# Performance work log

Measured on AMD Instinct MI355X. Metric: run time of the kernel, lower is better.

Reference implementation:

```python
import jax, jax.numpy as jnp
import numpy as np

S, B, C, H = 1024, 4, 1024, 16
CC = C // H


def setup_inputs() -> dict:
    key = jax.random.key(0)
    ks = jax.random.split(key, 10)
    scale = 1.0 / np.sqrt(C)
    return {
        "x": jax.random.normal(ks[0], (S, B, C), dtype=jnp.float32),
        "r": jax.random.normal(ks[1], (S, B, C), dtype=jnp.float32),
        "Wq": jax.random.normal(ks[2], (C, C), dtype=jnp.float32) * scale,
        "bq": jnp.zeros((C,), dtype=jnp.float32),
        "Wke": jax.random.normal(ks[3], (C, C), dtype=jnp.float32) * scale,
        "bke": jnp.zeros((C,), dtype=jnp.float32),
        "Wkr": jax.random.normal(ks[4], (C, C), dtype=jnp.float32) * scale,
        "bkr": jnp.zeros((C,), dtype=jnp.float32),
        "u": jax.random.normal(ks[5], (C,), dtype=jnp.float32) * 0.02,
        "v": jax.random.normal(ks[6], (C,), dtype=jnp.float32) * 0.02,
    }


def reference(x, r, Wq, bq, Wke, bke, Wkr, bkr, u, v):
    s, b, c = x.shape
    h, cc = H, CC
    # projections (torch Linear: y = x @ W^T + b)
    ewq = (x @ Wq.T + bq).reshape(s, b, h, cc)
    ewke_full = x @ Wke.T + bke                 # [s,b,c]
    ewke = ewke_full.reshape(s, b, h, cc)
    rwkr_full = r @ Wkr.T + bkr                 # [s,b,c]
    rwkr = rwkr_full.reshape(s, b, h, cc)
    # content-content and content-position terms
    term_a = jnp.einsum('sbnc,tbnc->stbn', ewq, ewke)
    term_b = jnp.einsum('sbnc,tbnc->stbn', ewq, rwkr)
    # global bias terms: uwke/vwke are constant over (s,b), so the stb einsum
    # reduces to a tb contraction broadcast over s (same math, no s*b copies)
    uwke = Wke @ u + bke                        # [c]
    vwke = Wkr @ v + bkr                        # [c]
    term_c = jnp.einsum('c,tbc->tb', uwke, ewke_full)   # [t,b]
    term_d = jnp.einsum('c,tbc->tb', vwke, rwkr_full)   # [t,b]
    bias = (term_c + term_d)[None, :, :, None]          # [1,t,b,1]
    return term_a + term_b + bias               # [s,t,b,h]
```

## Files before the change

### kernel.cpp

```cpp
#include <hip/hip_runtime.h>
#include <hip/hip_bf16.h>
#include <stdint.h>

#define Ssz 1024
#define Bsz 4
#define Csz 1024
#define Hsz 16
#define Msz 4096

typedef unsigned short u16;
typedef __attribute__((ext_vector_type(8))) short bf16x8;
typedef __attribute__((ext_vector_type(8))) unsigned short u16x8;
typedef __attribute__((ext_vector_type(4))) float f32x4;
typedef __attribute__((ext_vector_type(4))) unsigned short u16x4;

__device__ __forceinline__ u16 f2bf(float f) {
  union { float f; unsigned u; } x; x.f = f;
  unsigned r = x.u + 0x7fffu + ((x.u >> 16) & 1u);
  return (u16)(r >> 16);
}

__device__ __forceinline__ void glds16(const void* g, void* l) {
  __builtin_amdgcn_global_load_lds(
      (__attribute__((address_space(1))) void*)g,
      (__attribute__((address_space(3))) void*)l, 16, 0, 0);
}

__device__ __forceinline__ int swzb(int x) { return x ^ (((x >> 8) & 7) << 4); }

__global__ __launch_bounds__(256) void k_convert_w(
    const float* __restrict__ Wq, const float* __restrict__ Wke, const float* __restrict__ Wkr,
    const float* __restrict__ bke, const float* __restrict__ bkr,
    const float* __restrict__ uu, const float* __restrict__ vv,
    u16* __restrict__ Bq, u16* __restrict__ B2, float* __restrict__ biasK,
    float* __restrict__ uwke, float* __restrict__ vwke) {
  int c = blockIdx.x;
  int tid = threadIdx.x;
  int c4 = tid * 4;
  float4 q = *(const float4*)(Wq + (size_t)c * Csz + c4);
  float4 e = *(const float4*)(Wke + (size_t)c * Csz + c4);
  float4 k = *(const float4*)(Wkr + (size_t)c * Csz + c4);
  u16x4 qo = { f2bf(q.x), f2bf(q.y), f2bf(q.z), f2bf(q.w) };
  u16x4 eo = { f2bf(e.x), f2bf(e.y), f2bf(e.z), f2bf(e.w) };
  u16x4 ko = { f2bf(k.x), f2bf(k.y), f2bf(k.z), f2bf(k.w) };
  *(u16x4*)(Bq + (size_t)c * 1024 + c4) = qo;
  *(u16x4*)(B2 + (size_t)c * 2048 + c4) = eo;
  *(u16x4*)(B2 + (size_t)c * 2048 + 1024 + c4) = ko;
  float4 u4 = *(const float4*)(uu + c4);
  float4 v4 = *(const float4*)(vv + c4);
  float se = e.x * u4.x + e.y * u4.y + e.z * u4.z + e.w * u4.w;
  float sk = k.x * v4.x + k.y * v4.y + k.z * v4.z + k.w * v4.w;
  for (int m = 32; m; m >>= 1) { se += __shfl_xor(se, m); sk += __shfl_xor(sk, m); }
  __shared__ float red[2][4];
  if ((tid & 63) == 0) { red[0][tid >> 6] = se; red[1][tid >> 6] = sk; }
  __syncthreads();
  if (tid == 0) {
    uwke[c] = red[0][0] + red[0][1] + red[0][2] + red[0][3] + bke[c];
    vwke[c] = red[1][0] + red[1][1] + red[1][2] + red[1][3] + bkr[c];
    biasK[c] = bke[c] + bkr[c];
  }
}

__global__ __launch_bounds__(256) void k_prep2(
    const float* __restrict__ Wke, const float* __restrict__ Wkr,
    const float* __restrict__ uwke, const float* __restrict__ vwke,
    const float* __restrict__ bke, const float* __restrict__ bkr,
    float* __restrict__ wu, float* __restrict__ wv, float* __restrict__ cst) {
  int bid = blockIdx.x;
  int tid = threadIdx.x;
  if (bid < 64) {
    const float* W = (bid < 32) ? Wke : Wkr;
    const float* sv = (bid < 32) ? uwke : vwke;
    float* o = (bid < 32) ? wu : wv;
    int d = (bid & 31) * 32 + (tid & 31);
    int cpar = tid >> 5;
    float acc = 0.f;
    #pragma unroll 8
    for (int c = cpar; c < Csz; c += 8) acc += sv[c] * W[(size_t)c * Csz + d];
    __shared__ float red[8][32];
    red[cpar][tid & 31] = acc;
    __syncthreads();
    if (cpar == 0) {
      float s = 0.f;
      #pragma unroll
      for (int i = 0; i < 8; i++) s += red[i][tid & 31];
      o[d] = s;
    }
  } else {
    float s = 0.f;
    for (int i = tid; i < Csz; i += 256) s += uwke[i] * bke[i] + vwke[i] * bkr[i];
    for (int m = 32; m; m >>= 1) s += __shfl_xor(s, m);
    __shared__ float red1[4];
    if ((tid & 63) == 0) red1[tid >> 6] = s;
    __syncthreads();
    if (tid == 0) cst[0] = red1[0] + red1[1] + red1[2] + red1[3];
  }
}

__global__ __launch_bounds__(256) void k_convert_xr_bias(
    const float* __restrict__ x, const float* __restrict__ r,
    const float* __restrict__ wu, const float* __restrict__ wv,
    const float* __restrict__ cst, u16* __restrict__ A2, float* __restrict__ biasTB) {
  int m = blockIdx.x;
  int tid = threadIdx.x;
  int c4 = tid * 4;
  float4 xv = *(const float4*)(x + (size_t)m * Csz + c4);
  float4 rv = *(const float4*)(r + (size_t)m * Csz + c4);
  u16x4 xo = { f2bf(xv.x), f2bf(xv.y), f2bf(xv.z), f2bf(xv.w) };
  u16x4 ro = { f2bf(rv.x), f2bf(rv.y), f2bf(rv.z), f2bf(rv.w) };
  *(u16x4*)(A2 + (size_t)m * 2048 + c4) = xo;
  *(u16x4*)(A2 + (size_t)m * 2048 + 1024 + c4) = ro;
  float4 a = *(const float4*)(wu + c4);
  float4 b = *(const float4*)(wv + c4);
  float s = xv.x * a.x + xv.y * a.y + xv.z * a.z + xv.w * a.w
          + rv.x * b.x + rv.y * b.y + rv.z * b.z + rv.w * b.w;
  for (int mm = 32; mm; mm >>= 1) s += __shfl_xor(s, mm);
  __shared__ float red[4];
  if ((tid & 63) == 0) red[tid >> 6] = s;
  __syncthreads();
  if (tid == 0) biasTB[m] = red[0] + red[1] + red[2] + red[3] + cst[0];
}

__global__ __launch_bounds__(256, 4) void k_gemm(
    const u16* __restrict__ A2, const u16* __restrict__ Bq, const u16* __restrict__ B2,
    const float* __restrict__ bq, const float* __restrict__ biasK,
    u16* __restrict__ QF, u16* __restrict__ KF) {
  __shared__ char smem[32768];
  u16 (*As)[4096] = (u16(*)[4096])smem;
  u16 (*Bs)[4096] = (u16(*)[4096])(smem + 16384);
  u16* ep = (u16*)smem;

  const int z = blockIdx.z;
  const u16* A = A2; const int lda = 2048;
  const u16* B = (z == 0) ? Bq : B2;
  const int ldb = (z == 0) ? 1024 : 2048;
  const float* bias = (z == 0) ? bq : biasK;
  u16* OF = (z == 0) ? QF : KF;
  const int NT = ((z == 0) ? 1024 : 2048) >> 5;

  const int tid = threadIdx.x;
  const int bm = blockIdx.y * 128, bn = blockIdx.x * 128;
  const int wave = tid >> 6, lane = tid & 63;
  const int wm = (wave & 1) * 64, wn = (wave >> 1) * 64;
  const int fr = lane & 15, kg = (lane >> 4) * 8;

  const int ch0 = tid, ch1 = 256 + tid;
  const int r0 = ch0 >> 2, c0 = (ch0 & 3) * 8;
  const int r1 = ch1 >> 2, c1 = (ch1 & 3) * 8;
  const u16* a0 = A + (size_t)(bm + r0) * lda + c0;
  const u16* a1 = A + (size_t)(bm + r1) * lda + c1;
  const u16* b0 = B + (size_t)(bn + r0) * ldb + c0;
  const u16* b1 = B + (size_t)(bn + r1) * ldb + c1;

  f32x4 acc[4][4] = {};

  glds16(a0, &As[0][ch0 * 8]);  glds16(a1, &As[0][ch1 * 8]);
  glds16(b0, &Bs[0][ch0 * 8]);  glds16(b1, &Bs[0][ch1 * 8]);
  __syncthreads();

  for (int t = 0; t < NT; t++) {
    const int cur = t & 1;
    if (t + 1 < NT) {
      const int kt = (t + 1) * 32;
      glds16(a0 + kt, &As[cur ^ 1][ch0 * 8]);  glds16(a1 + kt, &As[cur ^ 1][ch1 * 8]);
      glds16(b0 + kt, &Bs[cur ^ 1][ch0 * 8]);  glds16(b1 + kt, &Bs[cur ^ 1][ch1 * 8]);
    }
    bf16x8 af[4], bf[4];
    #pragma unroll
    for (int mi = 0; mi < 4; mi++) af[mi] = *(const bf16x8*)(&As[cur][(wm + mi * 16 + fr) * 32 + kg]);
    #pragma unroll
    for (int ni = 0; ni < 4; ni++) bf[ni] = *(const bf16x8*)(&Bs[cur][(wn + ni * 16 + fr) * 32 + kg]);
    #pragma unroll
    for (int mi = 0; mi < 4; mi++)
      #pragma unroll
      for (int ni = 0; ni < 4; ni++)
        acc[mi][ni] = __builtin_amdgcn_mfma_f32_16x16x32_bf16(af[mi], bf[ni], acc[mi][ni], 0, 0, 0);
    __syncthreads();
  }

  const int hi = lane >> 4;
  const int e8 = fr & 7;
  const int fr3 = fr >> 3;
  u16* epw = ep + wave * 4096;
  float bvn[4];
  #pragma unroll
  for (int ni = 0; ni < 4; ni++) bvn[ni] = bias[bn + wn + ni * 16 + fr];
  #pragma unroll
  for (int ni = 0; ni < 4; ni++) {
    const int kk = ni >> 1;
    const int g = (ni * 2 + fr3) & 3;
    #pragma unroll
    for (int mi = 0; mi < 4; mi++) {
      const int inner = (g * 16 + mi * 4 + hi) * 8 + e8;
      #pragma unroll
      for (int j = 0; j < 4; j++)
        epw[(j * 2 + kk) * 512 + inner] = f2bf(acc[mi][ni][j] + bvn[ni]);
    }
  }
  const int s_tile = (bm >> 6) + (wm >> 6);
  const int nh = (bn + wn) >> 6;
  #pragma unroll
  for (int p = 0; p < 8; p++) {
    const int b2 = p >> 1, kk = p & 1;
    u16x8 v = *(const u16x8*)(&epw[p * 512 + lane * 8]);
    size_t ci = ((size_t)(s_tile * 4 + b2) * 16 + nh) * 2 + kk;
    *(u16x8*)(OF + ci * 512 + lane * 8) = v;
  }
}

__global__ __launch_bounds__(256, 3) void k_attn(
    const u16* __restrict__ QF, const u16* __restrict__ KF,
    const float* __restrict__ biasTB, float* __restrict__ out) {
  int id = blockIdx.x;
  int xcd = id & 7, within = id >> 3;
  int sx = xcd & 3, tx = xcd >> 2;
  int panel = within >> 7;
  int pl = within & 127;
  int s_tile = sx * 16 + (pl >> 3);
  int t_tile = tx * 32 + panel * 8 + (pl & 7);
  int s0 = s_tile * 16, t0 = t_tile * 16;

  int tid = threadIdx.x;
  int wave = tid >> 6, lane = tid & 63;
  int fr = lane & 15;

  const u16* qp = QF + (size_t)(s_tile * 4 + wave) * 16384 + lane * 8;
  const u16* kp = KF + (size_t)(t_tile * 4 + wave) * 16384 + lane * 8;

  f32x4 acc[16];
  #pragma unroll
  for (int n = 0; n < 16; n++) acc[n] = (f32x4){0.f, 0.f, 0.f, 0.f};

  #pragma unroll
  for (int n = 0; n < 16; n++) {
    #pragma unroll
    for (int kk = 0; kk < 2; kk++) {
      bf16x8 a  = *(const bf16x8*)(qp + (n * 2 + kk) * 512);
      bf16x8 bb = *(const bf16x8*)(kp + (n * 2 + kk) * 512);
      acc[n] = __builtin_amdgcn_mfma_f32_16x16x32_bf16(a, bb, acc[n], 0, 0, 0);
    }
  }

  __shared__ float lds[8192];
  float bv = biasTB[(t0 + (tid >> 4)) * 4 + ((tid >> 2) & 3)];
  int hi = (lane >> 4) & 1;
  int myg = (lane >> 4) >> 1;

  #pragma unroll
  for (int g = 0; g < 2; g++) {
    __syncthreads();
    if (myg == g) {
      #pragma unroll
      for (int j = 0; j < 4; j++) {
        int lbase = (((hi * 4 + j) * 16 + fr) * 4 + wave) * 64;
        #pragma unroll
        for (int n0 = 0; n0 < 16; n0 += 4) {
          f32x4 v = { acc[n0][j], acc[n0 + 1][j], acc[n0 + 2][j], acc[n0 + 3][j] };
          *(f32x4*)((char*)lds + swzb(lbase + n0 * 4)) = v;
        }
      }
    }
    __syncthreads();
    #pragma unroll
    for (int sr = 0; sr < 8; sr++) {
      f32x4 v = *(const f32x4*)((char*)lds + swzb(sr * 4096 + tid * 16));
      v += bv;
      size_t off = ((size_t)(s0 + g * 8 + sr) * 1024 + t0) * 64 + tid * 4;
      __builtin_nontemporal_store(v, (f32x4*)(out + off));
    }
  }
}

extern "C" void kernel_launch(void* const* d_in, const int* in_sizes, int n_in,
                              void* d_out, int out_size, void* d_ws, size_t ws_size,
                              hipStream_t stream) {
  const float* x   = (const float*)d_in[0];
  const float* r   = (const float*)d_in[1];
  const float* Wq  = (const float*)d_in[2];
  const float* bq  = (const float*)d_in[3];
  const float* Wke = (const float*)d_in[4];
  const float* bke = (const float*)d_in[5];
  const float* Wkr = (const float*)d_in[6];
  const float* bkr = (const float*)d_in[7];
  const float* uu  = (const float*)d_in[8];
  const float* vv  = (const float*)d_in[9];
  float* out = (float*)d_out;
  char* ws = (char*)d_ws;

  u16* A2 = (u16*)(ws + 0);
  u16* QF = (u16*)(ws + 16777216);
  u16* KF = (u16*)(ws + 25165824);
  u16* B2 = (u16*)(ws + 33554432);
  u16* Bq = (u16*)(ws + 37748736);
  float* uwke  = (float*)(ws + 39845888);
  float* vwke  = (float*)(ws + 39849984);
  float* wu    = (float*)(ws + 39854080);
  float* wv    = (float*)(ws + 39858176);
  float* biasK = (float*)(ws + 39862272);
  float* cst   = (float*)(ws + 39866368);
  float* biasTB = (float*)(ws + 39866624);

  k_convert_w<<<1024, 256, 0, stream>>>(Wq, Wke, Wkr, bke, bkr, uu, vv,
                                        Bq, B2, biasK, uwke, vwke);
  k_prep2<<<65, 256, 0, stream>>>(Wke, Wkr, uwke, vwke, bke, bkr, wu, wv, cst);
  k_convert_xr_bias<<<4096, 256, 0, stream>>>(x, r, wu, wv, cst, A2, biasTB);
  k_gemm<<<dim3(8, 32, 2), 256, 0, stream>>>(A2, Bq, B2, bq, biasK, QF, KF);
  k_attn<<<4096, 256, 0, stream>>>(QF, KF, biasTB, out);
}
```

Baseline: 130.0 us.

## Triple-buffer GEMM LDS tiles with explicit vmcnt waits and one barrier

Result: faster. 126.9 us (-2.4%).

```diff
diff --git a/kernel.cpp b/kernel.cpp
--- a/kernel.cpp
+++ b/kernel.cpp
@@ -121,14 +121,11 @@
   if (tid == 0) biasTB[m] = red[0] + red[1] + red[2] + red[3] + cst[0];
 }
 
-__global__ __launch_bounds__(256, 4) void k_gemm(
+__global__ __launch_bounds__(256, 3) void k_gemm(
     const u16* __restrict__ A2, const u16* __restrict__ Bq, const u16* __restrict__ B2,
     const float* __restrict__ bq, const float* __restrict__ biasK,
     u16* __restrict__ QF, u16* __restrict__ KF) {
-  __shared__ char smem[32768];
-  u16 (*As)[4096] = (u16(*)[4096])smem;
-  u16 (*Bs)[4096] = (u16(*)[4096])(smem + 16384);
-  u16* ep = (u16*)smem;
+  __shared__ u16 smem[24576];
 
   const int z = blockIdx.z;
   const u16* A = A2; const int lda = 2048;
@@ -154,34 +151,48 @@
 
   f32x4 acc[4][4] = {};
 
-  glds16(a0, &As[0][ch0 * 8]);  glds16(a1, &As[0][ch1 * 8]);
-  glds16(b0, &Bs[0][ch0 * 8]);  glds16(b1, &Bs[0][ch1 * 8]);
-  __syncthreads();
-
+  glds16(a0, smem + ch0 * 8);           glds16(a1, smem + ch1 * 8);
+  glds16(b0, smem + 4096 + ch0 * 8);    glds16(b1, smem + 4096 + ch1 * 8);
+  glds16(a0 + 32, smem + 8192 + ch0 * 8);        glds16(a1 + 32, smem + 8192 + ch1 * 8);
+  glds16(b0 + 32, smem + 8192 + 4096 + ch0 * 8); glds16(b1 + 32, smem + 8192 + 4096 + ch1 * 8);
+
+  int cur = 0;
   for (int t = 0; t < NT; t++) {
-    const int cur = t & 1;
-    if (t + 1 < NT) {
-      const int kt = (t + 1) * 32;
-      glds16(a0 + kt, &As[cur ^ 1][ch0 * 8]);  glds16(a1 + kt, &As[cur ^ 1][ch1 * 8]);
-      glds16(b0 + kt, &Bs[cur ^ 1][ch0 * 8]);  glds16(b1 + kt, &Bs[cur ^ 1][ch1 * 8]);
-    }
+    if (t == NT - 1) {
+      asm volatile("s_waitcnt vmcnt(0)" ::: "memory");
+    } else {
+      asm volatile("s_waitcnt vmcnt(4)" ::: "memory");
+    }
+    __builtin_amdgcn_s_barrier();
+    asm volatile("" ::: "memory");
+    if (t + 2 < NT) {
+      const int nxt = cur >= 1 ? cur - 1 : 2;
+      u16* an = smem + nxt * 8192;
+      u16* bn_ = an + 4096;
+      const int kt = (t + 2) * 32;
+      glds16(a0 + kt, an + ch0 * 8);   glds16(a1 + kt, an + ch1 * 8);
+      glds16(b0 + kt, bn_ + ch0 * 8);  glds16(b1 + kt, bn_ + ch1 * 8);
+    }
+    const u16* ac = smem + cur * 8192;
+    const u16* bc = ac + 4096;
     bf16x8 af[4], bf[4];
     #pragma unroll
-    for (int mi = 0; mi < 4; mi++) af[mi] = *(const bf16x8*)(&As[cur][(wm + mi * 16 + fr) * 32 + kg]);
-    #pragma unroll
-    for (int ni = 0; ni < 4; ni++) bf[ni] = *(const bf16x8*)(&Bs[cur][(wn + ni * 16 + fr) * 32 + kg]);
+    for (int mi = 0; mi < 4; mi++) af[mi] = *(const bf16x8*)(ac + (wm + mi * 16 + fr) * 32 + kg);
+    #pragma unroll
+    for (int ni = 0; ni < 4; ni++) bf[ni] = *(const bf16x8*)(bc + (wn + ni * 16 + fr) * 32 + kg);
     #pragma unroll
     for (int mi = 0; mi < 4; mi++)
       #pragma unroll
       for (int ni = 0; ni < 4; ni++)
         acc[mi][ni] = __builtin_amdgcn_mfma_f32_16x16x32_bf16(af[mi], bf[ni], acc[mi][ni], 0, 0, 0);
-    __syncthreads();
-  }
+    cur = cur < 2 ? cur + 1 : 0;
+  }
+  __syncthreads();
 
   const int hi = lane >> 4;
   const int e8 = fr & 7;
   const int fr3 = fr >> 3;
-  u16* epw = ep + wave * 4096;
+  u16* epw = smem + wave * 4096;
   float bvn[4];
   #pragma unroll
   for (int ni = 0; ni < 4; ni++) bvn[ni] = bias[bn + wn + ni * 16 + fr];
```
